# Kernel tuning notes

Hardware: AMD Instinct MI355X
Metric: run time of the kernel (lower is better)

Reference implementation:

```python
import jax, jax.numpy as jnp
import numpy as np

N, E = 50000, 800000
D, H, C, ED = 128, 8, 16, 4  # embed_dim, heads, head_dim, edge_dim


def _add_self_loops(edge_index, ea, n):
    # PyG add_self_loops with fill_value='mean': self-loop edge_attr is the
    # mean of incoming edge attributes per destination node (0 if none).
    src, dst = edge_index[0], edge_index[1]
    deg = jax.ops.segment_sum(jnp.ones((src.shape[0],), ea.dtype), dst, num_segments=n)
    loop_ea = jax.ops.segment_sum(ea, dst, num_segments=n) / jnp.maximum(deg, 1.0)[:, None]
    ar = jnp.arange(n, dtype=src.dtype)
    return (jnp.concatenate([src, ar]), jnp.concatenate([dst, ar]),
            jnp.concatenate([ea, loop_ea], axis=0))


def _gatv2(x, src, dst, ea, Wl, bl, Wr, br, We, att, bias, concat):
    n = x.shape[0]
    xl = (x @ Wl + bl).reshape(n, H, C)   # lin_l -> messages (source)
    xr = (x @ Wr + br).reshape(n, H, C)   # lin_r -> target
    e = (ea @ We).reshape(-1, H, C)       # lin_edge (no bias in PyG)
    m = jax.nn.leaky_relu(xl[src] + xr[dst] + e, negative_slope=0.2)  # [Etot,H,C]
    alpha = jnp.einsum('ehc,hc->eh', m, att)
    amax = jax.ops.segment_max(alpha, dst, num_segments=n)   # every node has a self loop
    ex = jnp.exp(alpha - amax[dst])
    den = jax.ops.segment_sum(ex, dst, num_segments=n)
    a = ex / den[dst]                                        # segment softmax over dst
    out = jax.ops.segment_sum(xl[src] * a[:, :, None], dst, num_segments=n)  # [N,H,C]
    out = out.reshape(n, H * C) if concat else out.mean(axis=1)
    return out + bias


def _ln(h, g, b):
    mu = h.mean(-1, keepdims=True)
    var = jnp.var(h, axis=-1, keepdims=True)
    return (h - mu) / jnp.sqrt(var + 1e-5) * g + b


def setup_inputs() -> dict:
    key = jax.random.key(0)
    ks = jax.random.split(key, 32)
    s = 0.05
    inp = {
        'x': jax.random.normal(ks[0], (N, D), jnp.float32),
        'edge_index': jax.random.randint(ks[1], (2, E), 0, N, jnp.int32),
        'edge_attr': jax.random.normal(ks[2], (E, ED), jnp.float32),
    }
    dims = [(D, H * C), (H * C, H * C), (H * C, C)]  # (in_dim, bias_dim per layer)
    k = 3
    for i, (din, bdim) in enumerate(dims):
        inp[f'Wl{i}'] = jax.random.normal(ks[k], (din, H * C), jnp.float32) * s; k += 1
        inp[f'bl{i}'] = jnp.zeros((H * C,), jnp.float32)
        inp[f'Wr{i}'] = jax.random.normal(ks[k], (din, H * C), jnp.float32) * s; k += 1
        inp[f'br{i}'] = jnp.zeros((H * C,), jnp.float32)
        inp[f'We{i}'] = jax.random.normal(ks[k], (ED, H * C), jnp.float32) * s; k += 1
        inp[f'att{i}'] = jax.random.normal(ks[k], (H, C), jnp.float32) * s; k += 1
        inp[f'b{i}'] = jnp.zeros((bdim,), jnp.float32)
        inp[f'g{i}'] = jnp.ones((bdim,), jnp.float32)
        inp[f'be{i}'] = jnp.zeros((bdim,), jnp.float32)
    inp['Wout'] = jax.random.normal(ks[k], (C, D), jnp.float32) * s
    inp['bout'] = jnp.zeros((D,), jnp.float32)
    return inp


def reference(x, edge_index, edge_attr,
              Wl0, bl0, Wr0, br0, We0, att0, b0, g0, be0,
              Wl1, bl1, Wr1, br1, We1, att1, b1, g1, be1,
              Wl2, bl2, Wr2, br2, We2, att2, b2, g2, be2,
              Wout, bout):
    n = x.shape[0]
    src, dst, ea = _add_self_loops(edge_index, edge_attr, n)
    layers = [
        (Wl0, bl0, Wr0, br0, We0, att0, b0, g0, be0, True),
        (Wl1, bl1, Wr1, br1, We1, att1, b1, g1, be1, True),
        (Wl2, bl2, Wr2, br2, We2, att2, b2, g2, be2, False),
    ]
    for (Wl, bl, Wr, br, We, att, bias, g, be, concat) in layers:
        h = _gatv2(x, src, dst, ea, Wl, bl, Wr, br, We, att, bias, concat)
        h = jax.nn.elu(h)
        h = _ln(h, g, be)
        if h.shape == x.shape:  # residual (layers 0,1)
            h = h + x
        x = h
    return x @ Wout + bout
```

## Files before the change

### kernel.cpp

```cpp
#include <hip/hip_runtime.h>
#include <hip/hip_bf16.h>

#define ND 128
#define NH 8
#define NC 16

typedef float v2f __attribute__((ext_vector_type(2)));
typedef short bf16x8 __attribute__((ext_vector_type(8)));
typedef float f32x4 __attribute__((ext_vector_type(4)));

static inline size_t alignup(size_t x){ return (x + 255) & ~size_t(255); }
__device__ __forceinline__ int imin(int a, int b){ return a < b ? a : b; }

__device__ __forceinline__ ushort f2bf(float f){
    __hip_bfloat16 h = __float2bfloat16(f);
    return *reinterpret_cast<ushort*>(&h);
}

__device__ __forceinline__ v2f unpack_bf2(uint u){
    v2f r;
    r.x = __uint_as_float(u << 16);
    r.y = __uint_as_float(u & 0xffff0000u);
    return r;
}

__device__ __forceinline__ v2f lrelu2(v2f z){
    v2f s = z * 0.2f;
    v2f r;
    r.x = fmaxf(z.x, s.x);
    r.y = fmaxf(z.y, s.y);
    return r;
}

__device__ __forceinline__ float hred8(float x){
    int y;
    y = __builtin_amdgcn_mov_dpp(__float_as_int(x), 0xB1, 0xF, 0xF, true);
    x += __int_as_float(y);
    y = __builtin_amdgcn_mov_dpp(__float_as_int(x), 0x4E, 0xF, 0xF, true);
    x += __int_as_float(y);
    y = __builtin_amdgcn_mov_dpp(__float_as_int(x), 0x141, 0xF, 0xF, true);
    x += __int_as_float(y);
    return x;
}


__global__ void hist_kernel(const int* __restrict__ dsts, int* __restrict__ deg, int E)
{
    int e = blockIdx.x * blockDim.x + threadIdx.x;
    if (e >= E) return;
    atomicAdd(&deg[dsts[e]], 1);
}

__global__ __launch_bounds__(1024) void scan_kernel(const int* __restrict__ deg,
                                                    int* __restrict__ rowstart, int n)
{
    __shared__ int wsum[16];
    int tid = threadIdx.x;
    int lane = tid & 63, wid = tid >> 6;
    int carry = 0;
    for (int base = 0; base < n; base += 4096) {
        int idx = base + tid * 4;
        int4 d = make_int4(0, 0, 0, 0);
        if (idx + 3 < n) d = *(const int4*)(deg + idx);
        else {
            if (idx < n)     d.x = deg[idx];
            if (idx + 1 < n) d.y = deg[idx + 1];
            if (idx + 2 < n) d.z = deg[idx + 2];
        }
        int p0 = (d.x + 3) & ~3, p1 = (d.y + 3) & ~3;
        int p2 = (d.z + 3) & ~3, p3 = (d.w + 3) & ~3;
        int tsum = p0 + p1 + p2 + p3;
        int s = tsum;
        #pragma unroll
        for (int o = 1; o < 64; o <<= 1) {
            int t = __shfl_up(s, o);
            if (lane >= o) s += t;
        }
        if (lane == 63) wsum[wid] = s;
        __syncthreads();
        int off = carry;
        #pragma unroll
        for (int w = 0; w < 16; ++w) {
            int ws_ = wsum[w];
            if (w < wid) off += ws_;
        }
        int total = 0;
        #pragma unroll
        for (int w = 0; w < 16; ++w) total += wsum[w];
        int excl = off + (s - tsum);
        if (idx < n)     rowstart[idx]     = excl;
        if (idx + 1 < n) rowstart[idx + 1] = excl + p0;
        if (idx + 2 < n) rowstart[idx + 2] = excl + p0 + p1;
        if (idx + 3 < n) rowstart[idx + 3] = excl + p0 + p1 + p2;
        carry += total;
        __syncthreads();
    }
    if (tid == 0) rowstart[n] = carry;
}

__global__ void scatter_kernel(const int* __restrict__ srcs, const int* __restrict__ dsts,
                               const float4* __restrict__ ea4,
                               const int* __restrict__ rowstart, int* __restrict__ cursor,
                               uint4* __restrict__ recs, int E)
{
    int e = blockIdx.x * blockDim.x + threadIdx.x;
    if (e >= E) return;
    int d = dsts[e];
    int pos = rowstart[d] + atomicAdd(&cursor[d], 1);
    float4 a = ea4[e];
    uint ea01 = (uint)f2bf(a.x) | ((uint)f2bf(a.y) << 16);
    uint ea23 = (uint)f2bf(a.z) | ((uint)f2bf(a.w) << 16);
    recs[pos] = make_uint4((uint)(srcs[e] << 8), ea01, ea23, 0u);
}

__global__ void padfill_kernel(const int* __restrict__ rowstart, const int* __restrict__ deg,
                               uint4* __restrict__ recs, int n)
{
    int v = blockIdx.x * blockDim.x + threadIdx.x;
    if (v < n) {
        int d = deg[v];
        int p = rowstart[v] + d;
        int pe = rowstart[v] + ((d + 3) & ~3);
        for (; p < pe; ++p) recs[p] = make_uint4(0u, 0u, 0u, 0u);
    } else if (v < n + 64) {
        int p = rowstart[n] + (v - n);
        recs[p] = make_uint4(0u, 0u, 0u, 0u);
    }
}

__global__ void easum_kernel(const int* __restrict__ rowstart, const int* __restrict__ deg,
                             const uint4* __restrict__ recs, float4* __restrict__ easum, int n)
{
    int v = blockIdx.x * blockDim.x + threadIdx.x;
    if (v >= n) return;
    int p0 = rowstart[v], d = deg[v];
    float sx = 0.f, sy = 0.f, sz = 0.f, sw = 0.f;
    for (int p = p0; p < p0 + d; ++p) {
        uint4 a = recs[p];
        sx += __uint_as_float(a.y << 16);
        sy += __uint_as_float(a.y & 0xffff0000u);
        sz += __uint_as_float(a.z << 16);
        sw += __uint_as_float(a.z & 0xffff0000u);
    }
    float inv = 1.0f / (float)(d > 0 ? d : 1);
    easum[v] = make_float4(sx * inv, sy * inv, sz * inv, sw * inv);
}


struct WSrc { const float* p[6]; };

__global__ void wconv_kernel(WSrc s, ushort* __restrict__ wt)
{
    int id = blockIdx.x * blockDim.x + threadIdx.x;
    int m = id >> 14;
    int r = id & 16383;
    int n = r >> 7, k = r & 127;
    wt[(size_t)m * 16384 + n * 128 + k] = f2bf(s.p[m][k * 128 + n]);
}


__global__ __launch_bounds__(256) void gemm_mfma(
    const float* __restrict__ X,
    const ushort* __restrict__ WTl, const float* __restrict__ bl,
    const ushort* __restrict__ WTr, const float* __restrict__ br,
    ushort* __restrict__ XLB, ushort* __restrict__ XRB, int nrows)
{
    __shared__ ushort xhi[64][136];
    __shared__ ushort xlo[64][136];
    int tid = threadIdx.x;
    int row0 = blockIdx.x * 64;

    const float4* X4 = (const float4*)X;
    #pragma unroll
    for (int i = tid; i < 64*32; i += 256) {
        int r = i >> 5, c = i & 31;
        float4 v = make_float4(0.f, 0.f, 0.f, 0.f);
        if (row0 + r < nrows) v = X4[(size_t)(row0 + r) * 32 + c];
        ushort4 h, l;
        h.x = f2bf(v.x); l.x = f2bf(v.x - __uint_as_float((uint)h.x << 16));
        h.y = f2bf(v.y); l.y = f2bf(v.y - __uint_as_float((uint)h.y << 16));
        h.z = f2bf(v.z); l.z = f2bf(v.z - __uint_as_float((uint)h.z << 16));
        h.w = f2bf(v.w); l.w = f2bf(v.w - __uint_as_float((uint)h.w << 16));
        *(ushort4*)&xhi[r][c * 4] = h;
        *(ushort4*)&xlo[r][c * 4] = l;
    }
    __syncthreads();

    int lane = tid & 63;
    int wid = tid >> 6;
    int c15 = lane & 15;
    int kblk = lane >> 4;
    int rowb = wid * 16;

    f32x4 accl[8], accr[8];
    #pragma unroll
    for (int nt = 0; nt < 8; ++nt) {
        float bvl = bl[nt * 16 + c15];
        float bvr = br[nt * 16 + c15];
        accl[nt] = (f32x4){bvl, bvl, bvl, bvl};
        accr[nt] = (f32x4){bvr, bvr, bvr, bvr};
    }

    const bf16x8* WL8 = (const bf16x8*)WTl;
    const bf16x8* WR8 = (const bf16x8*)WTr;

    #pragma unroll
    for (int kc = 0; kc < 4; ++kc) {
        int k0 = kc * 32 + kblk * 8;
        bf16x8 ahi = *(const bf16x8*)&xhi[rowb + c15][k0];
        bf16x8 alo = *(const bf16x8*)&xlo[rowb + c15][k0];
        int kidx = k0 >> 3;
        #pragma unroll
        for (int nt = 0; nt < 8; ++nt) {
            int bi = (nt * 16 + c15) * 16 + kidx;
            bf16x8 bfl = WL8[bi];
            bf16x8 bfr = WR8[bi];
            accl[nt] = __builtin_amdgcn_mfma_f32_16x16x32_bf16(ahi, bfl, accl[nt], 0, 0, 0);
            accl[nt] = __builtin_amdgcn_mfma_f32_16x16x32_bf16(alo, bfl, accl[nt], 0, 0, 0);
            accr[nt] = __builtin_amdgcn_mfma_f32_16x16x32_bf16(ahi, bfr, accr[nt], 0, 0, 0);
            accr[nt] = __builtin_amdgcn_mfma_f32_16x16x32_bf16(alo, bfr, accr[nt], 0, 0, 0);
        }
    }

    int crow = rowb + (lane >> 4) * 4;
    #pragma unroll
    for (int j = 0; j < 4; ++j) {
        int row = row0 + crow + j;
        if (row < nrows) {
            #pragma unroll
            for (int nt = 0; nt < 8; ++nt) {
                XLB[(size_t)row * 128 + nt * 16 + c15] = f2bf(accl[nt][j]);
                XRB[(size_t)row * 128 + nt * 16 + c15] = f2bf(accr[nt][j]);
            }
        }
    }
}


__device__ __forceinline__ void gat_wave(
    int dstv, int t,
    const uint* __restrict__ xl_u, const uint* __restrict__ xr_u,
    const int* __restrict__ rowstart, const int* __restrict__ deg,
    const uint4* __restrict__ recs, const float4* __restrict__ easum,
    v2f we0, v2f we1, v2f we2, v2f we3, v2f attv,
    v2f& r_out, float& l_out)
{
    v2f xrv = unpack_bf2(xr_u[(((uint)dstv) << 6) + t]);
    int p0 = __builtin_amdgcn_readfirstlane(rowstart[dstv]);
    int dv = __builtin_amdgcn_readfirstlane(deg[dstv]);
    int nb = (dv + 3) >> 2;
    int nbm1 = nb > 0 ? nb - 1 : 0;

    uint xsw = xl_u[(((uint)dstv) << 6) + t];

    const uint4* rp = recs + p0;
    const char* xlc = (const char*)xl_u;
    uint t4 = (uint)t * 4u;

    v2f a = {0.f, 0.f};
    float lsum = 0.f;

    uint4 rA0 = rp[0], rA1 = rp[1], rA2 = rp[2], rA3 = rp[3];
    int i1 = imin(1, nbm1) * 4;
    uint4 rB0 = rp[i1], rB1 = rp[i1+1], rB2 = rp[i1+2], rB3 = rp[i1+3];
    int i2 = imin(2, nbm1) * 4;
    uint4 rC0 = rp[i2], rC1 = rp[i2+1], rC2 = rp[i2+2], rC3 = rp[i2+3];

    uint gA0 = *(const uint*)(xlc + (rA0.x + t4));
    uint gA1 = *(const uint*)(xlc + (rA1.x + t4));
    uint gA2 = *(const uint*)(xlc + (rA2.x + t4));
    uint gA3 = *(const uint*)(xlc + (rA3.x + t4));
    uint gB0 = *(const uint*)(xlc + (rB0.x + t4));
    uint gB1 = *(const uint*)(xlc + (rB1.x + t4));
    uint gB2 = *(const uint*)(xlc + (rB2.x + t4));
    uint gB3 = *(const uint*)(xlc + (rB3.x + t4));

    for (int ib = 0; ib < nb; ++ib) {
        uint gC0 = *(const uint*)(xlc + (rC0.x + t4));
        uint gC1 = *(const uint*)(xlc + (rC1.x + t4));
        uint gC2 = *(const uint*)(xlc + (rC2.x + t4));
        uint gC3 = *(const uint*)(xlc + (rC3.x + t4));
        int i3 = imin(ib + 3, nbm1) * 4;
        uint4 rD0 = rp[i3], rD1 = rp[i3+1], rD2 = rp[i3+2], rD3 = rp[i3+3];

        float e0x = __uint_as_float(rA0.y << 16), e0y = __uint_as_float(rA0.y & 0xffff0000u);
        float e0z = __uint_as_float(rA0.z << 16), e0w = __uint_as_float(rA0.z & 0xffff0000u);
        float e1x = __uint_as_float(rA1.y << 16), e1y = __uint_as_float(rA1.y & 0xffff0000u);
        float e1z = __uint_as_float(rA1.z << 16), e1w = __uint_as_float(rA1.z & 0xffff0000u);
        float e2x = __uint_as_float(rA2.y << 16), e2y = __uint_as_float(rA2.y & 0xffff0000u);
        float e2z = __uint_as_float(rA2.z << 16), e2w = __uint_as_float(rA2.z & 0xffff0000u);
        float e3x = __uint_as_float(rA3.y << 16), e3y = __uint_as_float(rA3.y & 0xffff0000u);
        float e3z = __uint_as_float(rA3.z << 16), e3w = __uint_as_float(rA3.z & 0xffff0000u);

        v2f b0 = xrv + we0*e0x + we1*e0y + we2*e0z + we3*e0w;
        v2f b1 = xrv + we0*e1x + we1*e1y + we2*e1z + we3*e1w;
        v2f b2 = xrv + we0*e2x + we1*e2y + we2*e2z + we3*e2w;
        v2f b3 = xrv + we0*e3x + we1*e3y + we2*e3z + we3*e3w;

        v2f x0 = unpack_bf2(gA0);
        v2f x1 = unpack_bf2(gA1);
        v2f x2 = unpack_bf2(gA2);
        v2f x3 = unpack_bf2(gA3);

        v2f l0 = lrelu2(x0 + b0);
        v2f l1 = lrelu2(x1 + b1);
        v2f l2 = lrelu2(x2 + b2);
        v2f l3 = lrelu2(x3 + b3);

        v2f q0 = l0 * attv;
        v2f q1 = l1 * attv;
        v2f q2 = l2 * attv;
        v2f q3 = l3 * attv;
        float pt0 = q0.x + q0.y;
        float pt1 = q1.x + q1.y;
        float pt2 = q2.x + q2.y;
        float pt3 = q3.x + q3.y;

        if (ib == nb - 1) {
            int live = dv - ib*4;
            pt1 = (live > 1) ? pt1 : -1e30f;
            pt2 = (live > 2) ? pt2 : -1e30f;
            pt3 = (live > 3) ? pt3 : -1e30f;
        }

        float al0 = hred8(pt0);
        float al1 = hred8(pt1);
        float al2 = hred8(pt2);
        float al3 = hred8(pt3);

        float pe0 = exp2f(al0);
        float pe1 = exp2f(al1);
        float pe2 = exp2f(al2);
        float pe3 = exp2f(al3);
        lsum += (pe0 + pe1) + (pe2 + pe3);
        a += x0 * pe0;
        a += x1 * pe1;
        a += x2 * pe2;
        a += x3 * pe3;

        gA0 = gB0; gA1 = gB1; gA2 = gB2; gA3 = gB3;
        gB0 = gC0; gB1 = gC1; gB2 = gC2; gB3 = gC3;
        rA0 = rB0; rA1 = rB1; rA2 = rB2; rA3 = rB3;
        rB0 = rC0; rB1 = rC1; rB2 = rC2; rB3 = rC3;
        rC0 = rD0; rC1 = rD1; rC2 = rD2; rC3 = rD3;
    }

    float4 em = easum[dstv];
    v2f xs = unpack_bf2(xsw);
    v2f bs = xrv + we0*em.x + we1*em.y + we2*em.z + we3*em.w;
    v2f ls = lrelu2(xs + bs);
    v2f qs = ls * attv;
    float al = hred8(qs.x + qs.y);
    float pe = exp2f(al);
    l_out = lsum + pe;
    r_out = a + xs * pe;
}

__global__ __launch_bounds__(256) void attn_concat(
    const ushort* __restrict__ xlb, const ushort* __restrict__ xrb,
    const float* __restrict__ xin,
    const int* __restrict__ rowstart, const int* __restrict__ deg,
    const uint4* __restrict__ recs, const float4* __restrict__ easum,
    const float* __restrict__ We, const float* __restrict__ att,
    const float* __restrict__ bias, const float* __restrict__ g, const float* __restrict__ be,
    float* __restrict__ out, int n, int stride)
{
    int wid = threadIdx.x >> 6;
    int t = threadIdx.x & 63;

    v2f we0  = ((const v2f*)(We))[t];
    v2f we1  = ((const v2f*)(We + ND))[t];
    v2f we2  = ((const v2f*)(We + 2*ND))[t];
    v2f we3  = ((const v2f*)(We + 3*ND))[t];
    v2f attv = ((const v2f*)att)[t] * 1.44269504f;
    v2f bv   = ((const v2f*)bias)[t];
    v2f gv   = ((const v2f*)g)[t];
    v2f bev  = ((const v2f*)be)[t];

    for (int dstv = blockIdx.x * 4 + wid; dstv < n; dstv += stride) {
        v2f av; float l;
        gat_wave(dstv, t, (const uint*)xlb, (const uint*)xrb, rowstart, deg, recs, easum,
                 we0, we1, we2, we3, attv, av, l);

        float linv = 1.0f / l;
        v2f h = av * linv + bv;
        h.x = h.x > 0.f ? h.x : (__expf(h.x) - 1.0f);
        h.y = h.y > 0.f ? h.y : (__expf(h.y) - 1.0f);

        float ss = h.x + h.y, qq = h.x*h.x + h.y*h.y;
        #pragma unroll
        for (int o = 1; o < 64; o <<= 1) { ss += __shfl_xor(ss, o); qq += __shfl_xor(qq, o); }
        float mu = ss * (1.0f / ND);
        float var = qq * (1.0f / ND) - mu * mu;
        float rstd = rsqrtf(var + 1e-5f);

        v2f xiv = ((const v2f*)(xin + (size_t)dstv * ND))[t];
        v2f o2 = (h - mu) * rstd * gv + bev + xiv;
        ((v2f*)(out + (size_t)dstv * ND))[t] = o2;
    }
}

__global__ __launch_bounds__(256) void attn_final(
    const ushort* __restrict__ xlb, const ushort* __restrict__ xrb,
    const int* __restrict__ rowstart, const int* __restrict__ deg,
    const uint4* __restrict__ recs, const float4* __restrict__ easum,
    const float* __restrict__ We, const float* __restrict__ att,
    const float* __restrict__ b2, const float* __restrict__ g2, const float* __restrict__ be2,
    const float* __restrict__ Wout, const float* __restrict__ bout,
    float* __restrict__ out, int n, int stride)
{
    __shared__ float h16s[4][16];
    int wid = threadIdx.x >> 6;
    int t = threadIdx.x & 63;

    v2f we0  = ((const v2f*)(We))[t];
    v2f we1  = ((const v2f*)(We + ND))[t];
    v2f we2  = ((const v2f*)(We + 2*ND))[t];
    v2f we3  = ((const v2f*)(We + 3*ND))[t];
    v2f attv = ((const v2f*)att)[t] * 1.44269504f;
    int cc = t & 7;
    float2 b2v  = ((const float2*)b2)[cc];
    float2 g2v  = ((const float2*)g2)[cc];
    float2 be2v = ((const float2*)be2)[cc];
    float2 ov0  = ((const float2*)bout)[t];

    for (int dstv = blockIdx.x * 4 + wid; dstv < n; dstv += stride) {
        v2f av; float l;
        gat_wave(dstv, t, (const uint*)xlb, (const uint*)xrb, rowstart, deg, recs, easum,
                 we0, we1, we2, we3, attv, av, l);
        float linv = 1.0f / l;
        float v0 = av.x * linv, v1 = av.y * linv;

        #pragma unroll
        for (int o = 8; o < 64; o <<= 1) { v0 += __shfl_xor(v0, o); v1 += __shfl_xor(v1, o); }
        v0 = v0 * (1.0f / NH) + b2v.x;
        v1 = v1 * (1.0f / NH) + b2v.y;
        v0 = v0 > 0.f ? v0 : (__expf(v0) - 1.0f);
        v1 = v1 > 0.f ? v1 : (__expf(v1) - 1.0f);

        float ss = v0 + v1, qq = v0*v0 + v1*v1;
        #pragma unroll
        for (int o = 1; o < 8; o <<= 1) { ss += __shfl_xor(ss, o); qq += __shfl_xor(qq, o); }
        float mu = ss * (1.0f / NC);
        float var = qq * (1.0f / NC) - mu * mu;
        float rstd = rsqrtf(var + 1e-5f);
        float t0 = (v0 - mu) * rstd * g2v.x + be2v.x;
        float t1 = (v1 - mu) * rstd * g2v.y + be2v.y;

        if (t < 8) { h16s[wid][2*t] = t0; h16s[wid][2*t + 1] = t1; }

        float2 ov = ov0;
        #pragma unroll
        for (int k = 0; k < NC; k++) {
            float hk = h16s[wid][k];
            float2 wv = ((const float2*)Wout)[k * 64 + t];
            ov.x = fmaf(hk, wv.x, ov.x);
            ov.y = fmaf(hk, wv.y, ov.y);
        }
        ((float2*)(out + (size_t)dstv * ND))[t] = ov;
    }
}


extern "C" void kernel_launch(void* const* d_in, const int* in_sizes, int n_in,
                              void* d_out, int out_size, void* d_ws, size_t ws_size,
                              hipStream_t stream)
{
    const float* x_in = (const float*)d_in[0];
    const int*   ei   = (const int*)d_in[1];
    const float* ea   = (const float*)d_in[2];
    const int N = in_sizes[0] / ND;
    const int E = in_sizes[1] / 2;
    const int* srcs = ei;
    const int* dsts = ei + E;
    const float4* ea4 = (const float4*)ea;

    const float *Wl[3], *bl[3], *Wr[3], *br[3], *We[3], *att[3], *bb[3], *gg[3], *be[3];
    for (int l = 0; l < 3; l++) {
        int b = 3 + 9 * l;
        Wl[l]  = (const float*)d_in[b + 0];
        bl[l]  = (const float*)d_in[b + 1];
        Wr[l]  = (const float*)d_in[b + 2];
        br[l]  = (const float*)d_in[b + 3];
        We[l]  = (const float*)d_in[b + 4];
        att[l] = (const float*)d_in[b + 5];
        bb[l]  = (const float*)d_in[b + 6];
        gg[l]  = (const float*)d_in[b + 7];
        be[l]  = (const float*)d_in[b + 8];
    }
    const float* Wout = (const float*)d_in[30];
    const float* bout = (const float*)d_in[31];

    const size_t EP = (size_t)E + 3 * (size_t)N + 96;

    char* ws = (char*)d_ws;
    size_t off = 0;
    int* deg        = (int*)(ws + off);      off = alignup(off + (size_t)N * 4);
    int* cursor     = (int*)(ws + off);      off = alignup(off + (size_t)N * 4);
    size_t zero_bytes = off;
    int* rowstart   = (int*)(ws + off);      off = alignup(off + (size_t)(N + 1) * 4);
    uint4* recs     = (uint4*)(ws + off);    off = alignup(off + EP * 16);
    float4* easum   = (float4*)(ws + off);   off = alignup(off + (size_t)N * 16);
    ushort* xlb     = (ushort*)(ws + off);   off = alignup(off + (size_t)N * ND * 2);
    ushort* xrb     = (ushort*)(ws + off);   off = alignup(off + (size_t)N * ND * 2);
    float* xa       = (float*)(ws + off);    off = alignup(off + (size_t)N * ND * 4);
    ushort* wt      = (ushort*)(ws + off);   off = alignup(off + (size_t)6 * 16384 * 2);
    float* xb       = (float*)d_out;

    hipMemsetAsync(d_ws, 0, zero_bytes, stream);

    WSrc wsrc;
    wsrc.p[0] = Wl[0]; wsrc.p[1] = Wr[0];
    wsrc.p[2] = Wl[1]; wsrc.p[3] = Wr[1];
    wsrc.p[4] = Wl[2]; wsrc.p[5] = Wr[2];
    wconv_kernel<<<(6 * 16384) / 256, 256, 0, stream>>>(wsrc, wt);

    int ethreads = 256;
    int eblocks = (E + ethreads - 1) / ethreads;
    hist_kernel<<<eblocks, ethreads, 0, stream>>>(dsts, deg, E);
    scan_kernel<<<1, 1024, 0, stream>>>(deg, rowstart, N);
    padfill_kernel<<<(N + 64 + 255) / 256, 256, 0, stream>>>(rowstart, deg, recs, N);
    scatter_kernel<<<eblocks, ethreads, 0, stream>>>(srcs, dsts, ea4, rowstart, cursor, recs, E);
    easum_kernel<<<(N + 255) / 256, 256, 0, stream>>>(rowstart, deg, recs, easum, N);

    int gblocks = (N + 63) / 64;
    int ablocks = 2048;
    int astride = ablocks * 4;

    const ushort* WT0l = wt;
    const ushort* WT0r = wt + 16384;
    const ushort* WT1l = wt + 2 * 16384;
    const ushort* WT1r = wt + 3 * 16384;
    const ushort* WT2l = wt + 4 * 16384;
    const ushort* WT2r = wt + 5 * 16384;

    gemm_mfma<<<gblocks, 256, 0, stream>>>(x_in, WT0l, bl[0], WT0r, br[0], xlb, xrb, N);
    attn_concat<<<ablocks, 256, 0, stream>>>(xlb, xrb, x_in, rowstart, deg, recs, easum,
                                             We[0], att[0], bb[0], gg[0], be[0], xa, N, astride);
    gemm_mfma<<<gblocks, 256, 0, stream>>>(xa, WT1l, bl[1], WT1r, br[1], xlb, xrb, N);
    attn_concat<<<ablocks, 256, 0, stream>>>(xlb, xrb, xa, rowstart, deg, recs, easum,
                                             We[1], att[1], bb[1], gg[1], be[1], xb, N, astride);
    gemm_mfma<<<gblocks, 256, 0, stream>>>(xb, WT2l, bl[2], WT2r, br[2], xlb, xrb, N);
    attn_final<<<ablocks, 256, 0, stream>>>(xlb, xrb, rowstart, deg, recs, easum,
                                            We[2], att[2], bb[2], gg[2], be[2],
                                            Wout, bout, (float*)d_out, N, astride);
}
```

Measured before the change: 450.8 us.

## Merge preprocessing kernels, drop prefetch clamping, launch one wave per node

```diff
diff --git a/kernel.cpp b/kernel.cpp
--- a/kernel.cpp
+++ b/kernel.cpp
@@ -10,7 +10,6 @@
 typedef float f32x4 __attribute__((ext_vector_type(4)));
 
 static inline size_t alignup(size_t x){ return (x + 255) & ~size_t(255); }
-__device__ __forceinline__ int imin(int a, int b){ return a < b ? a : b; }
 
 __device__ __forceinline__ ushort f2bf(float f){
     __hip_bfloat16 h = __float2bfloat16(f);
@@ -44,11 +43,31 @@
 }
 
 
-__global__ void hist_kernel(const int* __restrict__ dsts, int* __restrict__ deg, int E)
-{
-    int e = blockIdx.x * blockDim.x + threadIdx.x;
-    if (e >= E) return;
-    atomicAdd(&deg[dsts[e]], 1);
+struct WSrc { const float* p[6]; };
+
+#define WTHREADS (6 * 16384)
+
+__global__ void prep_kernel(WSrc s, ushort* __restrict__ wt,
+                            const int* __restrict__ dsts, int* __restrict__ deg, int E)
+{
+    int id = blockIdx.x * blockDim.x + threadIdx.x;
+    if (id < WTHREADS) {
+        int m = id >> 14;
+        int r = id & 16383;
+        int n = r >> 7, k = r & 127;
+        wt[(size_t)m * 16384 + n * 128 + k] = f2bf(s.p[m][k * 128 + n]);
+    } else {
+        int e4 = (id - WTHREADS) * 4;
+        if (e4 + 3 < E) {
+            int4 d = *(const int4*)(dsts + e4);
+            atomicAdd(&deg[d.x], 1);
+            atomicAdd(&deg[d.y], 1);
+            atomicAdd(&deg[d.z], 1);
+            atomicAdd(&deg[d.w], 1);
+        } else if (e4 < E) {
+            for (int e = e4; e < E; ++e) atomicAdd(&deg[dsts[e]], 1);
+        }
+    }
 }
 
 __global__ __launch_bounds__(1024) void scan_kernel(const int* __restrict__ deg,
@@ -100,30 +119,25 @@
 
 __global__ void scatter_kernel(const int* __restrict__ srcs, const int* __restrict__ dsts,
                                const float4* __restrict__ ea4,
-                               const int* __restrict__ rowstart, int* __restrict__ cursor,
-                               uint4* __restrict__ recs, int E)
-{
-    int e = blockIdx.x * blockDim.x + threadIdx.x;
-    if (e >= E) return;
-    int d = dsts[e];
-    int pos = rowstart[d] + atomicAdd(&cursor[d], 1);
-    float4 a = ea4[e];
-    uint ea01 = (uint)f2bf(a.x) | ((uint)f2bf(a.y) << 16);
-    uint ea23 = (uint)f2bf(a.z) | ((uint)f2bf(a.w) << 16);
-    recs[pos] = make_uint4((uint)(srcs[e] << 8), ea01, ea23, 0u);
-}
-
-__global__ void padfill_kernel(const int* __restrict__ rowstart, const int* __restrict__ deg,
-                               uint4* __restrict__ recs, int n)
-{
-    int v = blockIdx.x * blockDim.x + threadIdx.x;
-    if (v < n) {
+                               const int* __restrict__ rowstart, const int* __restrict__ deg,
+                               int* __restrict__ cursor, uint4* __restrict__ recs, int E, int n)
+{
+    int id = blockIdx.x * blockDim.x + threadIdx.x;
+    if (id < E) {
+        int d = dsts[id];
+        int pos = rowstart[d] + atomicAdd(&cursor[d], 1);
+        float4 a = ea4[id];
+        recs[pos] = make_uint4((uint)(srcs[id] << 8),
+                               (uint)f2bf(a.x) | ((uint)f2bf(a.y) << 16),
+                               (uint)f2bf(a.z) | ((uint)f2bf(a.w) << 16), 0u);
+    } else if (id < E + n) {
+        int v = id - E;
         int d = deg[v];
         int p = rowstart[v] + d;
         int pe = rowstart[v] + ((d + 3) & ~3);
         for (; p < pe; ++p) recs[p] = make_uint4(0u, 0u, 0u, 0u);
-    } else if (v < n + 64) {
-        int p = rowstart[n] + (v - n);
+    } else if (id < E + n + 96) {
+        int p = rowstart[n] + (id - E - n);
         recs[p] = make_uint4(0u, 0u, 0u, 0u);
     }
 }
@@ -144,18 +158,6 @@
     }
     float inv = 1.0f / (float)(d > 0 ? d : 1);
     easum[v] = make_float4(sx * inv, sy * inv, sz * inv, sw * inv);
-}
-
-
-struct WSrc { const float* p[6]; };
-
-__global__ void wconv_kernel(WSrc s, ushort* __restrict__ wt)
-{
-    int id = blockIdx.x * blockDim.x + threadIdx.x;
-    int m = id >> 14;
-    int r = id & 16383;
-    int n = r >> 7, k = r & 127;
-    wt[(size_t)m * 16384 + n * 128 + k] = f2bf(s.p[m][k * 128 + n]);
 }
 
 
@@ -242,14 +244,19 @@
     const uint* __restrict__ xl_u, const uint* __restrict__ xr_u,
     const int* __restrict__ rowstart, const int* __restrict__ deg,
     const uint4* __restrict__ recs, const float4* __restrict__ easum,
-    v2f we0, v2f we1, v2f we2, v2f we3, v2f attv,
+    const float* __restrict__ We, const float* __restrict__ att,
     v2f& r_out, float& l_out)
 {
-    v2f xrv = unpack_bf2(xr_u[(((uint)dstv) << 6) + t]);
+    v2f we0  = ((const v2f*)(We))[t];
+    v2f we1  = ((const v2f*)(We + ND))[t];
+    v2f we2  = ((const v2f*)(We + 2*ND))[t];
+    v2f we3  = ((const v2f*)(We + 3*ND))[t];
+    v2f attv = ((const v2f*)att)[t] * 1.44269504f;
+    v2f xrv  = unpack_bf2(xr_u[(((uint)dstv) << 6) + t]);
+
     int p0 = __builtin_amdgcn_readfirstlane(rowstart[dstv]);
     int dv = __builtin_amdgcn_readfirstlane(deg[dstv]);
     int nb = (dv + 3) >> 2;
-    int nbm1 = nb > 0 ? nb - 1 : 0;
 
     uint xsw = xl_u[(((uint)dstv) << 6) + t];
 
@@ -260,28 +267,25 @@
     v2f a = {0.f, 0.f};
     float lsum = 0.f;
 
-    uint4 rA0 = rp[0], rA1 = rp[1], rA2 = rp[2], rA3 = rp[3];
-    int i1 = imin(1, nbm1) * 4;
-    uint4 rB0 = rp[i1], rB1 = rp[i1+1], rB2 = rp[i1+2], rB3 = rp[i1+3];
-    int i2 = imin(2, nbm1) * 4;
-    uint4 rC0 = rp[i2], rC1 = rp[i2+1], rC2 = rp[i2+2], rC3 = rp[i2+3];
-
-    uint gA0 = *(const uint*)(xlc + (rA0.x + t4));
-    uint gA1 = *(const uint*)(xlc + (rA1.x + t4));
-    uint gA2 = *(const uint*)(xlc + (rA2.x + t4));
-    uint gA3 = *(const uint*)(xlc + (rA3.x + t4));
-    uint gB0 = *(const uint*)(xlc + (rB0.x + t4));
-    uint gB1 = *(const uint*)(xlc + (rB1.x + t4));
-    uint gB2 = *(const uint*)(xlc + (rB2.x + t4));
-    uint gB3 = *(const uint*)(xlc + (rB3.x + t4));
+    uint4 rA0 = rp[0],  rA1 = rp[1],  rA2 = rp[2],  rA3 = rp[3];
+    uint4 rB0 = rp[4],  rB1 = rp[5],  rB2 = rp[6],  rB3 = rp[7];
+    uint4 rC0 = rp[8],  rC1 = rp[9],  rC2 = rp[10], rC3 = rp[11];
+    uint xA0 = *(const uint*)(xlc + (rA0.x + t4));
+    uint xA1 = *(const uint*)(xlc + (rA1.x + t4));
+    uint xA2 = *(const uint*)(xlc + (rA2.x + t4));
+    uint xA3 = *(const uint*)(xlc + (rA3.x + t4));
+    uint xB0 = *(const uint*)(xlc + (rB0.x + t4));
+    uint xB1 = *(const uint*)(xlc + (rB1.x + t4));
+    uint xB2 = *(const uint*)(xlc + (rB2.x + t4));
+    uint xB3 = *(const uint*)(xlc + (rB3.x + t4));
 
     for (int ib = 0; ib < nb; ++ib) {
-        uint gC0 = *(const uint*)(xlc + (rC0.x + t4));
-        uint gC1 = *(const uint*)(xlc + (rC1.x + t4));
-        uint gC2 = *(const uint*)(xlc + (rC2.x + t4));
-        uint gC3 = *(const uint*)(xlc + (rC3.x + t4));
-        int i3 = imin(ib + 3, nbm1) * 4;
-        uint4 rD0 = rp[i3], rD1 = rp[i3+1], rD2 = rp[i3+2], rD3 = rp[i3+3];
+        uint xC0 = *(const uint*)(xlc + (rC0.x + t4));
+        uint xC1 = *(const uint*)(xlc + (rC1.x + t4));
+        uint xC2 = *(const uint*)(xlc + (rC2.x + t4));
+        uint xC3 = *(const uint*)(xlc + (rC3.x + t4));
+        uint4 rD0 = rp[ib*4 + 12], rD1 = rp[ib*4 + 13];
+        uint4 rD2 = rp[ib*4 + 14], rD3 = rp[ib*4 + 15];
 
         float e0x = __uint_as_float(rA0.y << 16), e0y = __uint_as_float(rA0.y & 0xffff0000u);
         float e0z = __uint_as_float(rA0.z << 16), e0w = __uint_as_float(rA0.z & 0xffff0000u);
@@ -297,10 +301,10 @@
         v2f b2 = xrv + we0*e2x + we1*e2y + we2*e2z + we3*e2w;
         v2f b3 = xrv + we0*e3x + we1*e3y + we2*e3z + we3*e3w;
 
-        v2f x0 = unpack_bf2(gA0);
-        v2f x1 = unpack_bf2(gA1);
-        v2f x2 = unpack_bf2(gA2);
-        v2f x3 = unpack_bf2(gA3);
+        v2f x0 = unpack_bf2(xA0);
+        v2f x1 = unpack_bf2(xA1);
+        v2f x2 = unpack_bf2(xA2);
+        v2f x3 = unpack_bf2(xA3);
 
         v2f l0 = lrelu2(x0 + b0);
         v2f l1 = lrelu2(x1 + b1);
@@ -338,8 +342,8 @@
         a += x2 * pe2;
         a += x3 * pe3;
 
-        gA0 = gB0; gA1 = gB1; gA2 = gB2; gA3 = gB3;
-        gB0 = gC0; gB1 = gC1; gB2 = gC2; gB3 = gC3;
+        xA0 = xB0; xA1 = xB1; xA2 = xB2; xA3 = xB3;
+        xB0 = xC0; xB1 = xC1; xB2 = xC2; xB3 = xC3;
         rA0 = rB0; rA1 = rB1; rA2 = rB2; rA3 = rB3;
         rB0 = rC0; rB1 = rC1; rB2 = rC2; rB3 = rC3;
         rC0 = rD0; rC1 = rD1; rC2 = rD2; rC3 = rD3;
@@ -363,41 +367,35 @@
     const uint4* __restrict__ recs, const float4* __restrict__ easum,
     const float* __restrict__ We, const float* __restrict__ att,
     const float* __restrict__ bias, const float* __restrict__ g, const float* __restrict__ be,
-    float* __restrict__ out, int n, int stride)
+    float* __restrict__ out, int n)
 {
     int wid = threadIdx.x >> 6;
     int t = threadIdx.x & 63;
-
-    v2f we0  = ((const v2f*)(We))[t];
-    v2f we1  = ((const v2f*)(We + ND))[t];
-    v2f we2  = ((const v2f*)(We + 2*ND))[t];
-    v2f we3  = ((const v2f*)(We + 3*ND))[t];
-    v2f attv = ((const v2f*)att)[t] * 1.44269504f;
-    v2f bv   = ((const v2f*)bias)[t];
-    v2f gv   = ((const v2f*)g)[t];
-    v2f bev  = ((const v2f*)be)[t];
-
-    for (int dstv = blockIdx.x * 4 + wid; dstv < n; dstv += stride) {
-        v2f av; float l;
-        gat_wave(dstv, t, (const uint*)xlb, (const uint*)xrb, rowstart, deg, recs, easum,
-                 we0, we1, we2, we3, attv, av, l);
-
-        float linv = 1.0f / l;
-        v2f h = av * linv + bv;
-        h.x = h.x > 0.f ? h.x : (__expf(h.x) - 1.0f);
-        h.y = h.y > 0.f ? h.y : (__expf(h.y) - 1.0f);
-
-        float ss = h.x + h.y, qq = h.x*h.x + h.y*h.y;
-        #pragma unroll
-        for (int o = 1; o < 64; o <<= 1) { ss += __shfl_xor(ss, o); qq += __shfl_xor(qq, o); }
-        float mu = ss * (1.0f / ND);
-        float var = qq * (1.0f / ND) - mu * mu;
-        float rstd = rsqrtf(var + 1e-5f);
-
-        v2f xiv = ((const v2f*)(xin + (size_t)dstv * ND))[t];
-        v2f o2 = (h - mu) * rstd * gv + bev + xiv;
-        ((v2f*)(out + (size_t)dstv * ND))[t] = o2;
-    }
+    int dstv = blockIdx.x * 4 + wid;
+    if (dstv >= n) return;
+
+    v2f av; float l;
+    gat_wave(dstv, t, (const uint*)xlb, (const uint*)xrb, rowstart, deg, recs, easum,
+             We, att, av, l);
+
+    v2f bv = ((const v2f*)bias)[t];
+    float linv = 1.0f / l;
+    v2f h = av * linv + bv;
+    h.x = h.x > 0.f ? h.x : (__expf(h.x) - 1.0f);
+    h.y = h.y > 0.f ? h.y : (__expf(h.y) - 1.0f);
+
+    float ss = h.x + h.y, qq = h.x*h.x + h.y*h.y;
+    #pragma unroll
+    for (int o = 1; o < 64; o <<= 1) { ss += __shfl_xor(ss, o); qq += __shfl_xor(qq, o); }
+    float mu = ss * (1.0f / ND);
+    float var = qq * (1.0f / ND) - mu * mu;
+    float rstd = rsqrtf(var + 1e-5f);
+
+    v2f gv  = ((const v2f*)g)[t];
+    v2f bev = ((const v2f*)be)[t];
+    v2f xiv = ((const v2f*)(xin + (size_t)dstv * ND))[t];
+    v2f o2 = (h - mu) * rstd * gv + bev + xiv;
+    ((v2f*)(out + (size_t)dstv * ND))[t] = o2;
 }
 
 __global__ __launch_bounds__(256) void attn_final(
@@ -407,58 +405,51 @@
     const float* __restrict__ We, const float* __restrict__ att,
     const float* __restrict__ b2, const float* __restrict__ g2, const float* __restrict__ be2,
     const float* __restrict__ Wout, const float* __restrict__ bout,
-    float* __restrict__ out, int n, int stride)
+    float* __restrict__ out, int n)
 {
     __shared__ float h16s[4][16];
     int wid = threadIdx.x >> 6;
     int t = threadIdx.x & 63;
-
-    v2f we0  = ((const v2f*)(We))[t];
-    v2f we1  = ((const v2f*)(We + ND))[t];
-    v2f we2  = ((const v2f*)(We + 2*ND))[t];
-    v2f we3  = ((const v2f*)(We + 3*ND))[t];
-    v2f attv = ((const v2f*)att)[t] * 1.44269504f;
+    int dstv = blockIdx.x * 4 + wid;
+    if (dstv >= n) return;
+
+    v2f av; float l;
+    gat_wave(dstv, t, (const uint*)xlb, (const uint*)xrb, rowstart, deg, recs, easum,
+             We, att, av, l);
+    float linv = 1.0f / l;
+    float v0 = av.x * linv, v1 = av.y * linv;
+
+    #pragma unroll
+    for (int o = 8; o < 64; o <<= 1) { v0 += __shfl_xor(v0, o); v1 += __shfl_xor(v1, o); }
     int cc = t & 7;
-    float2 b2v  = ((const float2*)b2)[cc];
-    float2 g2v  = ((const float2*)g2)[cc];
+    float2 b2v = ((const float2*)b2)[cc];
+    v0 = v0 * (1.0f / NH) + b2v.x;
+    v1 = v1 * (1.0f / NH) + b2v.y;
+    v0 = v0 > 0.f ? v0 : (__expf(v0) - 1.0f);
+    v1 = v1 > 0.f ? v1 : (__expf(v1) - 1.0f);
+
+    float ss = v0 + v1, qq = v0*v0 + v1*v1;
+    #pragma unroll
+    for (int o = 1; o < 8; o <<= 1) { ss += __shfl_xor(ss, o); qq += __shfl_xor(qq, o); }
+    float mu = ss * (1.0f / NC);
+    float var = qq * (1.0f / NC) - mu * mu;
+    float rstd = rsqrtf(var + 1e-5f);
+    float2 g2v = ((const float2*)g2)[cc];
     float2 be2v = ((const float2*)be2)[cc];
-    float2 ov0  = ((const float2*)bout)[t];
-
-    for (int dstv = blockIdx.x * 4 + wid; dstv < n; dstv += stride) {
-        v2f av; float l;
-        gat_wave(dstv, t, (const uint*)xlb, (const uint*)xrb, rowstart, deg, recs, easum,
-                 we0, we1, we2, we3, attv, av, l);
-        float linv = 1.0f / l;
-        float v0 = av.x * linv, v1 = av.y * linv;
-
-        #pragma unroll
-        for (int o = 8; o < 64; o <<= 1) { v0 += __shfl_xor(v0, o); v1 += __shfl_xor(v1, o); }
-        v0 = v0 * (1.0f / NH) + b2v.x;
-        v1 = v1 * (1.0f / NH) + b2v.y;
-        v0 = v0 > 0.f ? v0 : (__expf(v0) - 1.0f);
-        v1 = v1 > 0.f ? v1 : (__expf(v1) - 1.0f);
-
-        float ss = v0 + v1, qq = v0*v0 + v1*v1;
-        #pragma unroll
-        for (int o = 1; o < 8; o <<= 1) { ss += __shfl_xor(ss, o); qq += __shfl_xor(qq, o); }
-        float mu = ss * (1.0f / NC);
-        float var = qq * (1.0f / NC) - mu * mu;
-        float rstd = rsqrtf(var + 1e-5f);
-        float t0 = (v0 - mu) * rstd * g2v.x + be2v.x;
-        float t1 = (v1 - mu) * rstd * g2v.y + be2v.y;
-
-        if (t < 8) { h16s[wid][2*t] = t0; h16s[wid][2*t + 1] = t1; }
-
-        float2 ov = ov0;
-        #pragma unroll
-        for (int k = 0; k < NC; k++) {
-            float hk = h16s[wid][k];
-            float2 wv = ((const float2*)Wout)[k * 64 + t];
-            ov.x = fmaf(hk, wv.x, ov.x);
-            ov.y = fmaf(hk, wv.y, ov.y);
-        }
-        ((float2*)(out + (size_t)dstv * ND))[t] = ov;
-    }
+    float t0 = (v0 - mu) * rstd * g2v.x + be2v.x;
+    float t1 = (v1 - mu) * rstd * g2v.y + be2v.y;
+
+    if (t < 8) { h16s[wid][2*t] = t0; h16s[wid][2*t + 1] = t1; }
+
+    float2 ov = ((const float2*)bout)[t];
+    #pragma unroll
+    for (int k = 0; k < NC; k++) {
+        float hk = h16s[wid][k];
+        float2 wv = ((const float2*)Wout)[k * 64 + t];
+        ov.x = fmaf(hk, wv.x, ov.x);
+        ov.y = fmaf(hk, wv.y, ov.y);
+    }
+    ((float2*)(out + (size_t)dstv * ND))[t] = ov;
 }
 
 
@@ -513,19 +504,17 @@
     wsrc.p[0] = Wl[0]; wsrc.p[1] = Wr[0];
     wsrc.p[2] = Wl[1]; wsrc.p[3] = Wr[1];
     wsrc.p[4] = Wl[2]; wsrc.p[5] = Wr[2];
-    wconv_kernel<<<(6 * 16384) / 256, 256, 0, stream>>>(wsrc, wt);
-
-    int ethreads = 256;
-    int eblocks = (E + ethreads - 1) / ethreads;
-    hist_kernel<<<eblocks, ethreads, 0, stream>>>(dsts, deg, E);
+
+    int pthreads = WTHREADS + (E + 3) / 4;
+    prep_kernel<<<(pthreads + 255) / 256, 256, 0, stream>>>(wsrc, wt, dsts, deg, E);
     scan_kernel<<<1, 1024, 0, stream>>>(deg, rowstart, N);
-    padfill_kernel<<<(N + 64 + 255) / 256, 256, 0, stream>>>(rowstart, deg, recs, N);
-    scatter_kernel<<<eblocks, ethreads, 0, stream>>>(srcs, dsts, ea4, rowstart, cursor, recs, E);
+    int sthreads = E + N + 96;
+    scatter_kernel<<<(sthreads + 255) / 256, 256, 0, stream>>>(srcs, dsts, ea4, rowstart, deg,
+                                                               cursor, recs, E, N);
     easum_kernel<<<(N + 255) / 256, 256, 0, stream>>>(rowstart, deg, recs, easum, N);
 
     int gblocks = (N + 63) / 64;
-    int ablocks = 2048;
-    int astride = ablocks * 4;
+    int ablocks = (N + 3) / 4;
 
     const ushort* WT0l = wt;
     const ushort* WT0r = wt + 16384;
@@ -536,12 +525,12 @@
 
     gemm_mfma<<<gblocks, 256, 0, stream>>>(x_in, WT0l, bl[0], WT0r, br[0], xlb, xrb, N);
     attn_concat<<<ablocks, 256, 0, stream>>>(xlb, xrb, x_in, rowstart, deg, recs, easum,
-                                             We[0], att[0], bb[0], gg[0], be[0], xa, N, astride);
+                                             We[0], att[0], bb[0], gg[0], be[0], xa, N);
     gemm_mfma<<<gblocks, 256, 0, stream>>>(xa, WT1l, bl[1], WT1r, br[1], xlb, xrb, N);
     attn_concat<<<ablocks, 256, 0, stream>>>(xlb, xrb, xa, rowstart, deg, recs, easum,
-                                             We[1], att[1], bb[1], gg[1], be[1], xb, N, astride);
+                                             We[1], att[1], bb[1], gg[1], be[1], xb, N);
     gemm_mfma<<<gblocks, 256, 0, stream>>>(xb, WT2l, bl[2], WT2r, br[2], xlb, xrb, N);
     attn_final<<<ablocks, 256, 0, stream>>>(xlb, xrb, rowstart, deg, recs, easum,
                                             We[2], att[2], bb[2], gg[2], be[2],
-                                            Wout, bout, (float*)d_out, N, astride);
-}
+                                            Wout, bout, (float*)d_out, N);
+}
```

Result: faster. 418.9 us, median of 2 (-7.1%).
